# Optimization experiments

Hardware: AMD Instinct MI355X
Metric: run time of the kernel (lower is better)

The kernel has to match this reference:

```python
import jax, jax.numpy as jnp
import numpy as np
import math

B, S, E, H = 2, 2048, 1024, 16
D = E // H  # d_attn = 64
SCALE = 1.0 / math.sqrt(D)


def setup_inputs() -> dict:
    key = jax.random.key(0)
    ks = jax.random.split(key, 5)
    std = 0.02
    return {
        "q": jax.random.normal(ks[0], (B, S, E), dtype=jnp.float32),
        "Wq": jax.random.normal(ks[1], (E, H * D), dtype=jnp.float32) * std,
        "Wk": jax.random.normal(ks[2], (E, H * D), dtype=jnp.float32) * std,
        "Wv": jax.random.normal(ks[3], (E, H * D), dtype=jnp.float32) * std,
        "Wo": jax.random.normal(ks[4], (H * D, E), dtype=jnp.float32) * std,
        "gamma": jnp.ones((H,), dtype=jnp.float32),
    }


def reference(q, Wq, Wk, Wv, Wo, gamma):
    Bq, Sq, _ = q.shape
    # projections -> [B, H, S, D]
    qh = (q @ Wq).reshape(Bq, Sq, H, D).transpose(0, 2, 1, 3)
    kh = (q @ Wk).reshape(Bq, Sq, H, D).transpose(0, 2, 1, 3)
    vh = (q @ Wv).reshape(Bq, Sq, H, D).transpose(0, 2, 1, 3)
    # RBF distance scores: ||q||^2 - 2 q.k + ||k||^2, clamped at 0
    q_norm = jnp.sum(qh * qh, axis=-1, keepdims=True)          # [B,H,S,1]
    k_norm = jnp.sum(kh * kh, axis=-1, keepdims=True)          # [B,H,S,1]
    qk = jnp.einsum("bhsd,bhtd->bhst", qh, kh)                # [B,H,S,S]
    dist = jnp.maximum(q_norm - 2.0 * qk + jnp.swapaxes(k_norm, -2, -1), 0.0)
    scores = jnp.exp(-gamma[None, :, None, None] * SCALE * dist)
    # source: masked_fill(causal_mask == 0, 0) with mask = triu(ones, 1)
    # -> scores kept only on the STRICT upper triangle (faithful to source)
    mask = jnp.triu(jnp.ones((Sq, Sq), dtype=bool), k=1)
    scores = jnp.where(mask, scores, 0.0)
    out = jnp.einsum("bhst,bhtd->bhsd", scores, vh)            # [B,H,S,D]
    out = out.transpose(0, 2, 1, 3).reshape(Bq, Sq, H * D)
    return out @ Wo
```

## Files before the change

### kernel.cpp

```cpp
#include <hip/hip_runtime.h>
#include <stdint.h>

#define SCALE 0.125f
#define GSL_C 0.180336880111f

typedef short s16x8 __attribute__((ext_vector_type(8)));
typedef float f32x4 __attribute__((ext_vector_type(4)));
typedef float f32x16 __attribute__((ext_vector_type(16)));

__device__ __forceinline__ unsigned short f2bf(float x){
  union { float f; unsigned int u; } v; v.f = x;
  unsigned int r = v.u + 0x7fffu + ((v.u >> 16) & 1u);
  return (unsigned short)(r >> 16);
}
__device__ __forceinline__ float bf2f(unsigned short u){
  union { unsigned int u; float f; } v; v.u = ((unsigned int)u) << 16;
  return v.f;
}
__device__ __forceinline__ f32x4 mfma16(s16x8 a, s16x8 b, f32x4 c){
  return __builtin_amdgcn_mfma_f32_16x16x32_bf16(a, b, c, 0, 0, 0);
}
__device__ __forceinline__ f32x16 mfma32(s16x8 a, s16x8 b, f32x16 c){
  return __builtin_amdgcn_mfma_f32_32x32x16_bf16(a, b, c, 0, 0, 0);
}
__device__ __forceinline__ void gld_lds16(const void* g, void* l){
  __builtin_amdgcn_global_load_lds(
      (const __attribute__((address_space(1))) unsigned int*)g,
      (__attribute__((address_space(3))) unsigned int*)l, 16, 0, 0);
}
__device__ __forceinline__ unsigned int cvtpk(float lo, float hi){
  unsigned int r;
  asm("v_cvt_pk_bf16_f32 %0, %1, %2" : "=v"(r) : "v"(lo), "v"(hi));
  return r;
}
__device__ __forceinline__ void plswap(unsigned int &a, unsigned int &b){
  asm("v_permlane32_swap_b32 %0, %1" : "+v"(a), "+v"(b));
}

__global__ __launch_bounds__(256) void prep_kernel(const float* __restrict__ in,
    unsigned short* __restrict__ out,
    const float* __restrict__ W0, const float* __restrict__ W1,
    const float* __restrict__ W2, const float* __restrict__ W3,
    unsigned short* __restrict__ Wt){
  int bid = blockIdx.x;
  int tid = threadIdx.x;
  if (bid < 2048){
    int i = bid*256 + tid;
    const float4* p = (const float4*)in + (size_t)i*2;
    float4 a = p[0], b = p[1];
    unsigned short t[8] = {f2bf(a.x),f2bf(a.y),f2bf(a.z),f2bf(a.w),
                           f2bf(b.x),f2bf(b.y),f2bf(b.z),f2bf(b.w)};
    *(s16x8*)(out + (size_t)i*8) = *(const s16x8*)t;
  } else {
    int idx = bid - 2048;
    int z = idx >> 8, rem = idx & 255;
    int k0 = (rem & 15)*64, n0 = (rem >> 4)*64;
    const float* src = (z==0)?W0:(z==1)?W1:(z==2)?W2:W3;
    unsigned short* dst = Wt + (size_t)z*1048576;
    __shared__ unsigned short tile[64*72];
    int r = tid>>2, c = (tid&3)*16;
    const float* p = src + (size_t)(k0+r)*1024 + n0 + c;
    #pragma unroll
    for (int j=0;j<16;j++) tile[r*72 + c + j] = f2bf(p[j]);
    __syncthreads();
    int n = tid>>2, kc = (tid&3)*16;
    unsigned short o[16];
    #pragma unroll
    for (int j=0;j<16;j++) o[j] = tile[(kc+j)*72 + n];
    *(s16x8*)&dst[(size_t)(n0+n)*1024 + k0 + kc]     = *(const s16x8*)o;
    *(s16x8*)&dst[(size_t)(n0+n)*1024 + k0 + kc + 8] = *(const s16x8*)(o+8);
  }
}

__global__ __launch_bounds__(256) void vtrans_kernel(const unsigned short* __restrict__ Vh,
    unsigned short* __restrict__ VtG){
  int bh = blockIdx.y, t0 = blockIdx.x*64;
  __shared__ unsigned short tile[64*72];
  int tid = threadIdx.x;
  #pragma unroll
  for (int p=0;p<2;p++){
    int idx = p*2048 + tid*8;
    int r = idx>>6, c = idx&63;
    *(s16x8*)&tile[r*72 + c] = *(const s16x8*)&Vh[((size_t)bh*2048 + t0 + r)*64 + c];
  }
  __syncthreads();
  #pragma unroll
  for (int p=0;p<2;p++){
    int idx = p*2048 + tid*8;
    int d = idx>>6, c = idx&63;
    unsigned short o[8];
    #pragma unroll
    for (int j=0;j<8;j++) o[j] = tile[(c+j)*72 + d];
    *(s16x8*)&VtG[((size_t)bh*64 + d)*2048 + t0 + c] = *(const s16x8*)o;
  }
}

template<int MODE>
__global__ __launch_bounds__(512) void gemm_db(const unsigned short* __restrict__ A,
    const unsigned short* __restrict__ Bt, unsigned short* __restrict__ outH,
    float* __restrict__ outF, float* __restrict__ qn, float* __restrict__ kn,
    const float* __restrict__ gamma){
  __shared__ short As[16384];
  __shared__ short Bs[16384];
  int tid = threadIdx.x;
  int w = tid>>6, l = tid&63;
  int lm = l & 15, hi = l >> 4;
  int wr = w>>1, wc = w&1;
  int m0 = blockIdx.x*128, n0 = blockIdx.y*128;

  const unsigned short* Bz;
  int bn0;
  if constexpr (MODE==1){ Bz = Bt + (size_t)(n0>>10)*1048576; bn0 = n0 & 1023; }
  else                  { Bz = Bt; bn0 = n0; }

  f32x4 acc[2][4];
  #pragma unroll
  for (int r=0;r<2;r++)
    #pragma unroll
    for (int c=0;c<4;c++){ f32x4 z = {0.f,0.f,0.f,0.f}; acc[r][c] = z; }

  int rsub = l>>3, csw = ((l&7) ^ (l>>3))*8;
  const unsigned short* gA = A  + (size_t)(m0  + w*16 + rsub)*1024 + csw;
  const unsigned short* gB = Bz + (size_t)(bn0 + w*16 + rsub)*1024 + csw;
  short* lA = As + w*1024;
  short* lB = Bs + w*1024;

  int ch0 = ((hi)     ^ (lm&7))*8;
  int ch1 = ((4 + hi) ^ (lm&7))*8;

  gld_lds16(gA,        lA);
  gld_lds16(gA + 8192, lA + 512);
  gld_lds16(gB,        lB);
  gld_lds16(gB + 8192, lB + 512);
  __syncthreads();

  const int NKT = 16;
  int buf = 0;
  for (int kt=0; kt<NKT; ++kt){
    if (kt+1 < NKT){
      const unsigned short* a = gA + (size_t)(kt+1)*64;
      const unsigned short* b = gB + (size_t)(kt+1)*64;
      short* dA = As + (buf^1)*8192 + w*1024;
      short* dB = Bs + (buf^1)*8192 + w*1024;
      gld_lds16(a,        dA);
      gld_lds16(a + 8192, dA + 512);
      gld_lds16(b,        dB);
      gld_lds16(b + 8192, dB + 512);
    }
    const short* curA = As + buf*8192;
    const short* curB = Bs + buf*8192;
    s16x8 af[2][2], bfv[4][2];
    #pragma unroll
    for (int r=0;r<2;r++){
      int ro = (wr*32 + r*16 + lm)*64;
      af[r][0] = *(const s16x8*)(curA + ro + ch0);
      af[r][1] = *(const s16x8*)(curA + ro + ch1);
    }
    #pragma unroll
    for (int c=0;c<4;c++){
      int ro = (wc*64 + c*16 + lm)*64;
      bfv[c][0] = *(const s16x8*)(curB + ro + ch0);
      bfv[c][1] = *(const s16x8*)(curB + ro + ch1);
    }
    __builtin_amdgcn_s_setprio(1);
    #pragma unroll
    for (int s=0;s<2;s++)
      #pragma unroll
      for (int r=0;r<2;r++)
        #pragma unroll
        for (int c=0;c<4;c++)
          acc[r][c] = mfma16(af[r][s], bfv[c][s], acc[r][c]);
    __builtin_amdgcn_s_setprio(0);
    __syncthreads();
    buf ^= 1;
  }

  if constexpr (MODE==0){
    #pragma unroll
    for (int r=0;r<2;r++)
      #pragma unroll
      for (int c=0;c<4;c++)
        #pragma unroll
        for (int i=0;i<4;i++){
          int m = m0 + wr*32 + r*16 + hi*4 + i;
          int n = n0 + wc*64 + c*16 + lm;
          outF[(size_t)m*1024 + n] = acc[r][c][i];
        }
  } else {
    int z = n0 >> 10;
    unsigned short* oz = outH + (size_t)z*4194304;
    #pragma unroll
    for (int r=0;r<2;r++){
      #pragma unroll
      for (int i=0;i<4;i++){
        int m = m0 + wr*32 + r*16 + hi*4 + i;
        int bq = m >> 11, sq = m & 2047;
        float nrm = 0.f;
        #pragma unroll
        for (int c=0;c<4;c++){
          int nn = (n0 & 1023) + wc*64 + c*16 + lm;
          int hq = nn >> 6, dq = nn & 63;
          int bh = bq*16 + hq;
          unsigned short bv = f2bf(acc[r][c][i]);
          oz[((size_t)bh*2048 + sq)*64 + dq] = bv;
          float vf = bf2f(bv);
          nrm = fmaf(vf, vf, nrm);
        }
        if (z < 2){
          nrm += __shfl_xor(nrm, 1);
          nrm += __shfl_xor(nrm, 2);
          nrm += __shfl_xor(nrm, 4);
          nrm += __shfl_xor(nrm, 8);
          if (lm == 0){
            int hq = ((n0 & 1023) + wc*64) >> 6;
            float gsl_h = gamma[hq] * GSL_C;
            float* dst = z ? kn : qn;
            dst[(size_t)(bq*16 + hq)*2048 + sq] = nrm * gsl_h;
          }
        }
      }
    }
  }
}

__global__ __launch_bounds__(512) void gemm_out(const unsigned short* __restrict__ A,
    const unsigned short* __restrict__ Bt, float* __restrict__ outF){
  __shared__ short As[16384];
  __shared__ short Bs[8192];
  int tid = threadIdx.x;
  int w = tid>>6, l = tid&63;
  int lm = l & 15, hi = l >> 4;
  int wr = w>>1, wc = w&1;
  int m0 = blockIdx.x*128, n0 = blockIdx.y*64;

  f32x4 acc[2][2];
  #pragma unroll
  for (int r=0;r<2;r++)
    #pragma unroll
    for (int c=0;c<2;c++){ f32x4 z = {0.f,0.f,0.f,0.f}; acc[r][c] = z; }

  int rsub = l>>3, csw = ((l&7) ^ (l>>3))*8;
  const unsigned short* gA = A  + (size_t)(m0 + w*16 + rsub)*1024 + csw;
  const unsigned short* gB = Bt + (size_t)(n0 + w*8  + rsub)*1024 + csw;

  int ch0 = ((hi)     ^ (lm&7))*8;
  int ch1 = ((4 + hi) ^ (lm&7))*8;

  gld_lds16(gA,        As + w*1024);
  gld_lds16(gA + 8192, As + w*1024 + 512);
  gld_lds16(gB,        Bs + w*512);
  __syncthreads();

  const int NKT = 16;
  int buf = 0;
  for (int kt=0; kt<NKT; ++kt){
    if (kt+1 < NKT){
      const unsigned short* a = gA + (size_t)(kt+1)*64;
      const unsigned short* b = gB + (size_t)(kt+1)*64;
      gld_lds16(a,        As + (buf^1)*8192 + w*1024);
      gld_lds16(a + 8192, As + (buf^1)*8192 + w*1024 + 512);
      gld_lds16(b,        Bs + (buf^1)*4096 + w*512);
    }
    const short* curA = As + buf*8192;
    const short* curB = Bs + buf*4096;
    s16x8 af[2][2], bfv[2][2];
    #pragma unroll
    for (int r=0;r<2;r++){
      int ro = (wr*32 + r*16 + lm)*64;
      af[r][0] = *(const s16x8*)(curA + ro + ch0);
      af[r][1] = *(const s16x8*)(curA + ro + ch1);
    }
    #pragma unroll
    for (int c=0;c<2;c++){
      int ro = (wc*32 + c*16 + lm)*64;
      bfv[c][0] = *(const s16x8*)(curB + ro + ch0);
      bfv[c][1] = *(const s16x8*)(curB + ro + ch1);
    }
    __builtin_amdgcn_s_setprio(1);
    #pragma unroll
    for (int s=0;s<2;s++)
      #pragma unroll
      for (int r=0;r<2;r++)
        #pragma unroll
        for (int c=0;c<2;c++)
          acc[r][c] = mfma16(af[r][s], bfv[c][s], acc[r][c]);
    __builtin_amdgcn_s_setprio(0);
    __syncthreads();
    buf ^= 1;
  }

  #pragma unroll
  for (int r=0;r<2;r++)
    #pragma unroll
    for (int c=0;c<2;c++)
      #pragma unroll
      for (int i=0;i<4;i++){
        int m = m0 + wr*32 + r*16 + hi*4 + i;
        int n = n0 + wc*32 + c*16 + lm;
        outF[(size_t)m*1024 + n] = acc[r][c][i];
      }
}

#define JOB(si,ts,te,buf,zm) ((unsigned int)((si)|((ts)<<4)|((te)<<10)|((buf)<<16)|((zm)<<18)))
__device__ const unsigned int JOBS[32] = {
  JOB(0,0,11,0,0),   JOB(5,10,21,0,0),  JOB(0,22,32,2,0),  JOB(1,12,22,1,0),
  JOB(2,4,14,0,0),   JOB(6,22,32,1,2),  JOB(2,23,32,2,0),  JOB(7,14,23,0,0),
  JOB(0,11,22,1,0),  JOB(5,21,32,1,2),  JOB(1,2,12,0,0),   JOB(1,22,32,2,0),
  JOB(6,12,22,0,0),  JOB(2,14,23,1,0),  JOB(3,6,15,0,0),   JOB(7,23,32,1,2),
  JOB(11,22,32,0,3), JOB(3,24,32,2,0),  JOB(4,8,16,0,0),   JOB(4,16,24,1,0),
  JOB(4,24,32,2,0),  JOB(8,16,24,0,0),  JOB(3,15,24,1,0),  JOB(8,24,32,1,2),
  JOB(15,30,32,0,3), JOB(14,28,32,0,3), JOB(10,20,26,0,0), JOB(10,26,32,1,2),
  JOB(13,26,32,0,3), JOB(9,18,25,0,0),  JOB(9,25,32,1,2),  JOB(12,24,32,0,3)
};

__global__ __launch_bounds__(256, 4) void attn_kernel(const unsigned short* __restrict__ Qh,
    const unsigned short* __restrict__ Kh, const unsigned short* __restrict__ VtG,
    const float* __restrict__ qn, const float* __restrict__ kn,
    const float* __restrict__ gamma, unsigned short* __restrict__ aO0,
    unsigned short* __restrict__ aO1, unsigned short* __restrict__ aO2){
  __shared__ short Ks[2][4096];
  __shared__ short Vs[2][4096];

  int bid = blockIdx.x;
  int bh = bid & 31; int b = bh>>4, h = bh&15;
  unsigned int e = JOBS[bid >> 5];
  int si2 = e & 15, ts = (e>>4)&63, te = (e>>10)&63, bsel = (e>>16)&3, zm = (e>>18)&3;
  int s0 = si2*128;

  int tid = threadIdx.x, w = tid>>6, l = tid&63;
  int l31 = l & 31, hi5 = l >> 5, l7 = l & 7;
  float gs2l = 2.f * gamma[h] * GSL_C;

  int q0 = s0 + w*32;
  int qrow = q0 + l31;
  const unsigned short* qb = Qh + ((size_t)bh*2048 + qrow)*64;
  s16x8 qf[4];
  #pragma unroll
  for (int c=0;c<4;c++) qf[c] = *(const s16x8*)(qb + c*16 + hi5*8);
  float gq = -qn[(size_t)bh*2048 + qrow];
  const float* knp = kn + (size_t)bh*2048;

  int chs = (l7 ^ (l>>3))*8;
  const unsigned short* kp0 = Kh  + ((size_t)bh*2048 + w*8 + (l>>3))*64 + chs;
  const unsigned short* vp0 = VtG + ((size_t)bh*64 + w*8 + (l>>3))*2048 + chs;

  f32x16 accO0, accO1;
  #pragma unroll
  for (int r=0;r<16;r++){ accO0[r] = 0.f; accO1[r] = 0.f; }

#define STAGE(bufi, tabs) { \
    const unsigned short* kp = kp0 + (size_t)(tabs)*64; \
    const unsigned short* vp = vp0 + (tabs); \
    short* dK = &Ks[bufi][w*512]; \
    short* dV = &Vs[bufi][w*512]; \
    gld_lds16(kp,           dK); \
    gld_lds16(kp + 32*64,   dK + 2048); \
    gld_lds16(vp,           dV); \
    gld_lds16(vp + 32*2048, dV + 2048); \
  }

  STAGE(0, ts*64);
  __syncthreads();

  int cur = 0;
  for (int tt = ts; tt < te; ++tt, cur ^= 1){
    int t0 = tt*64;
    float4 kv[8];
    #pragma unroll
    for (int j=0;j<8;j++) kv[j] = *(const float4*)(knp + t0 + j*8 + hi5*4);
    if (tt + 1 < te) STAGE(cur^1, (tt+1)*64);
    const short* kb = &Ks[cur][0];
    const short* vb = &Vs[cur][0];

    #pragma unroll
    for (int tb=0; tb<2; tb++){
      int tbase = t0 + tb*32 - s0;
      if (tbase + 31 <= w*32) continue;
      f32x16 sc;
      #pragma unroll
      for (int r=0;r<16;r++) sc[r] = 0.f;
      __builtin_amdgcn_s_setprio(1);
      #pragma unroll
      for (int c=0;c<4;c++){
        s16x8 kf = *(const s16x8*)(kb + (tb*32 + l31)*64 + (((2*c + hi5) ^ l7)*8));
        sc = mfma32(kf, qf[c], sc);
      }
      __builtin_amdgcn_s_setprio(0);
      float ev[16];
      #pragma unroll
      for (int gg=0; gg<4; gg++){
        float4 knv = kv[tb*4 + gg];
        float ks4[4] = {knv.x, knv.y, knv.z, knv.w};
        #pragma unroll
        for (int i=0;i<4;i++){
          int r = gg*4 + i;
          ev[r] = __builtin_amdgcn_exp2f(fminf(fmaf(gs2l, sc[r], gq - ks4[i]), 0.f));
        }
      }
      if (tbase < w*32 + 32){
        #pragma unroll
        for (int r=0;r<16;r++){
          int t = t0 + tb*32 + (r&3) + 8*(r>>2) + 4*hi5;
          ev[r] = (t > qrow) ? ev[r] : 0.f;
        }
      }
      unsigned int u0 = cvtpk(ev[0],  ev[1]),  u1 = cvtpk(ev[2],  ev[3]);
      unsigned int u2 = cvtpk(ev[4],  ev[5]),  u3 = cvtpk(ev[6],  ev[7]);
      unsigned int u4 = cvtpk(ev[8],  ev[9]),  u5 = cvtpk(ev[10], ev[11]);
      unsigned int u6 = cvtpk(ev[12], ev[13]), u7 = cvtpk(ev[14], ev[15]);
      plswap(u0, u2);
      plswap(u1, u3);
      plswap(u4, u6);
      plswap(u5, u7);
      unsigned int f0[4] = {u0, u1, u2, u3};
      unsigned int f1[4] = {u4, u5, u6, u7};
      s16x8 pa0 = *(const s16x8*)f0;
      s16x8 pa1 = *(const s16x8*)f1;
      __builtin_amdgcn_s_setprio(1);
      {
        int cg0 = 2*tb, cg1 = 2*tb + 1;
        s16x8 v00 = *(const s16x8*)(vb + (l31)*64      + (((2*cg0 + hi5) ^ l7)*8));
        s16x8 v01 = *(const s16x8*)(vb + (l31)*64      + (((2*cg1 + hi5) ^ l7)*8));
        s16x8 v10 = *(const s16x8*)(vb + (32 + l31)*64 + (((2*cg0 + hi5) ^ l7)*8));
        s16x8 v11 = *(const s16x8*)(vb + (32 + l31)*64 + (((2*cg1 + hi5) ^ l7)*8));
        accO0 = mfma32(pa0, v00, accO0);
        accO0 = mfma32(pa1, v01, accO0);
        accO1 = mfma32(pa0, v10, accO1);
        accO1 = mfma32(pa1, v11, accO1);
      }
      __builtin_amdgcn_s_setprio(0);
    }
    __syncthreads();
  }
#undef STAGE

  unsigned short* aoP = (bsel==0) ? aO0 : (bsel==1) ? aO1 : aO2;
  #pragma unroll
  for (int r=0;r<16;r++){
    int s = q0 + (r&3) + 8*(r>>2) + 4*hi5;
    size_t base = ((size_t)b*2048 + s)*1024 + h*64;
    aoP[base + l31]      = f2bf(accO0[r]);
    aoP[base + 32 + l31] = f2bf(accO1[r]);
  }
  if (zm){
    s16x8 zz8 = {0,0,0,0,0,0,0,0};
    int zr = tid >> 1, zc = (tid & 1)*32;
    size_t zbase = ((size_t)b*2048 + s0 + zr)*1024 + h*64 + zc;
    if (zm & 1){
      #pragma unroll
      for (int j=0;j<4;j++) *(s16x8*)&aO1[zbase + j*8] = zz8;
    }
    if (zm & 2){
      #pragma unroll
      for (int j=0;j<4;j++) *(s16x8*)&aO2[zbase + j*8] = zz8;
    }
  }
}

__global__ __launch_bounds__(256) void sum3_kernel(unsigned short* __restrict__ a,
    const unsigned short* __restrict__ bsrc, const unsigned short* __restrict__ csrc){
  size_t i = ((size_t)blockIdx.x*256 + threadIdx.x)*8;
  s16x8 va = *(const s16x8*)(a + i);
  s16x8 vb = *(const s16x8*)(bsrc + i);
  s16x8 vc = *(const s16x8*)(csrc + i);
  unsigned short o[8];
  #pragma unroll
  for (int j=0;j<8;j++)
    o[j] = f2bf(bf2f((unsigned short)va[j]) + bf2f((unsigned short)vb[j])
                + bf2f((unsigned short)vc[j]));
  *(s16x8*)(a + i) = *(const s16x8*)o;
}

extern "C" void kernel_launch(void* const* d_in, const int* in_sizes, int n_in,
                              void* d_out, int out_size, void* d_ws, size_t ws_size,
                              hipStream_t stream){
  const float* q  = (const float*)d_in[0];
  const float* Wq = (const float*)d_in[1];
  const float* Wk = (const float*)d_in[2];
  const float* Wv = (const float*)d_in[3];
  const float* Wo = (const float*)d_in[4];
  const float* gm = (const float*)d_in[5];
  float* out = (float*)d_out;

  unsigned short* qbf = (unsigned short*)d_ws;
  unsigned short* Wt  = qbf + 4194304;
  unsigned short* Qh  = Wt  + 4194304;
  unsigned short* Kh  = Qh  + 4194304;
  unsigned short* Vh  = Kh  + 4194304;
  unsigned short* Vt  = Vh  + 4194304;
  unsigned short* aO  = Vt  + 4194304;
  float* qn = (float*)(aO + 4194304);
  float* kn = qn + 65536;

  unsigned short* aO1 = qbf;
  unsigned short* aO2 = Vh;

  prep_kernel  <<<dim3(3072), 256, 0, stream>>>(q, qbf, Wq, Wk, Wv, Wo, Wt);
  gemm_db<1>   <<<dim3(32,24), 512, 0, stream>>>(qbf, Wt, Qh, nullptr, qn, kn, gm);
  vtrans_kernel<<<dim3(32,32), 256, 0, stream>>>(Vh, Vt);
  attn_kernel  <<<dim3(1024), 256, 0, stream>>>(Qh, Kh, Vt, qn, kn, gm, aO, aO1, aO2);
  sum3_kernel  <<<dim3(2048), 256, 0, stream>>>(aO, aO1, aO2);
  gemm_out     <<<dim3(32,16), 512, 0, stream>>>(aO, Wt + 3*1048576, out);
}
```

Measured before the change: 106.1 us.

## Fuse partial-sum reduction into output GEMM and rework projection GEMM with 32x32 MFMA split-K

Removes the separate sum3 kernel by having gemm_out load the three bf16 partial attention outputs, sum them in registers, and write the result into LDS while the MFMAs for the current tile run. The projection GEMM is rewritten to use 32x32x16 MFMAs with a two-way intra-block split-K across warp groups, reduced through LDS before the bf16 store and norm computation. This saves a kernel launch and one full read/write pass over the attention output, and should improve MFMA efficiency in the projection GEMM. In exchange it adds register pressure, an extra LDS exchange and sync, and non-async global loads in the output GEMM's A path.

```diff
diff --git a/kernel.cpp b/kernel.cpp
--- a/kernel.cpp
+++ b/kernel.cpp
@@ -95,135 +95,131 @@
   }
 }
 
-template<int MODE>
-__global__ __launch_bounds__(512) void gemm_db(const unsigned short* __restrict__ A,
+__global__ __launch_bounds__(512, 4) void gemm_proj(const unsigned short* __restrict__ A,
     const unsigned short* __restrict__ Bt, unsigned short* __restrict__ outH,
-    float* __restrict__ outF, float* __restrict__ qn, float* __restrict__ kn,
-    const float* __restrict__ gamma){
-  __shared__ short As[16384];
-  __shared__ short Bs[16384];
+    float* __restrict__ qn, float* __restrict__ kn, const float* __restrict__ gamma){
+  __shared__ short As[2][8192];
+  __shared__ short Bs[2][8192];
   int tid = threadIdx.x;
   int w = tid>>6, l = tid&63;
-  int lm = l & 15, hi = l >> 4;
-  int wr = w>>1, wc = w&1;
+  int l31 = l & 31, hi5 = l >> 5;
+  int wm = (w>>1)&1, wn = w&1, ks = w>>2, pid = w&3;
   int m0 = blockIdx.x*128, n0 = blockIdx.y*128;
-
-  const unsigned short* Bz;
-  int bn0;
-  if constexpr (MODE==1){ Bz = Bt + (size_t)(n0>>10)*1048576; bn0 = n0 & 1023; }
-  else                  { Bz = Bt; bn0 = n0; }
-
-  f32x4 acc[2][4];
-  #pragma unroll
-  for (int r=0;r<2;r++)
-    #pragma unroll
-    for (int c=0;c<4;c++){ f32x4 z = {0.f,0.f,0.f,0.f}; acc[r][c] = z; }
-
-  int rsub = l>>3, csw = ((l&7) ^ (l>>3))*8;
+  int z = n0 >> 10, bn0 = n0 & 1023;
+  const unsigned short* Bz = Bt + (size_t)z*1048576;
+
+  f32x16 acc[2][2];
+  #pragma unroll
+  for (int mh=0;mh<2;mh++)
+    #pragma unroll
+    for (int nh=0;nh<2;nh++)
+      #pragma unroll
+      for (int r=0;r<16;r++) acc[mh][nh][r] = 0.f;
+
+  int rsub = l>>3, csw = ((l&7) ^ rsub)*8;
   const unsigned short* gA = A  + (size_t)(m0  + w*16 + rsub)*1024 + csw;
   const unsigned short* gB = Bz + (size_t)(bn0 + w*16 + rsub)*1024 + csw;
-  short* lA = As + w*1024;
-  short* lB = Bs + w*1024;
-
-  int ch0 = ((hi)     ^ (lm&7))*8;
-  int ch1 = ((4 + hi) ^ (lm&7))*8;
-
-  gld_lds16(gA,        lA);
-  gld_lds16(gA + 8192, lA + 512);
-  gld_lds16(gB,        lB);
-  gld_lds16(gB + 8192, lB + 512);
+
+  int ch0 = ((4*ks + hi5)     ^ (l31&7))*8;
+  int ch1 = ((4*ks + 2 + hi5) ^ (l31&7))*8;
+
+  gld_lds16(gA,        &As[0][w*1024]);
+  gld_lds16(gA + 8192, &As[0][w*1024 + 512]);
+  gld_lds16(gB,        &Bs[0][w*1024]);
+  gld_lds16(gB + 8192, &Bs[0][w*1024 + 512]);
   __syncthreads();
 
-  const int NKT = 16;
   int buf = 0;
-  for (int kt=0; kt<NKT; ++kt){
-    if (kt+1 < NKT){
+  #pragma unroll 1
+  for (int kt=0; kt<16; ++kt){
+    if (kt+1 < 16){
       const unsigned short* a = gA + (size_t)(kt+1)*64;
       const unsigned short* b = gB + (size_t)(kt+1)*64;
-      short* dA = As + (buf^1)*8192 + w*1024;
-      short* dB = Bs + (buf^1)*8192 + w*1024;
-      gld_lds16(a,        dA);
-      gld_lds16(a + 8192, dA + 512);
-      gld_lds16(b,        dB);
-      gld_lds16(b + 8192, dB + 512);
-    }
-    const short* curA = As + buf*8192;
-    const short* curB = Bs + buf*8192;
-    s16x8 af[2][2], bfv[4][2];
-    #pragma unroll
-    for (int r=0;r<2;r++){
-      int ro = (wr*32 + r*16 + lm)*64;
-      af[r][0] = *(const s16x8*)(curA + ro + ch0);
-      af[r][1] = *(const s16x8*)(curA + ro + ch1);
-    }
-    #pragma unroll
-    for (int c=0;c<4;c++){
-      int ro = (wc*64 + c*16 + lm)*64;
-      bfv[c][0] = *(const s16x8*)(curB + ro + ch0);
-      bfv[c][1] = *(const s16x8*)(curB + ro + ch1);
+      gld_lds16(a,        &As[buf^1][w*1024]);
+      gld_lds16(a + 8192, &As[buf^1][w*1024 + 512]);
+      gld_lds16(b,        &Bs[buf^1][w*1024]);
+      gld_lds16(b + 8192, &Bs[buf^1][w*1024 + 512]);
+    }
+    const short* cA = &As[buf][0];
+    const short* cB = &Bs[buf][0];
+    s16x8 af[2][2], bfv[2][2];
+    #pragma unroll
+    for (int mh=0;mh<2;mh++){
+      int ro = (wm*64 + mh*32 + l31)*64;
+      af[mh][0] = *(const s16x8*)(cA + ro + ch0);
+      af[mh][1] = *(const s16x8*)(cA + ro + ch1);
+    }
+    #pragma unroll
+    for (int nh=0;nh<2;nh++){
+      int ro = (wn*64 + nh*32 + l31)*64;
+      bfv[nh][0] = *(const s16x8*)(cB + ro + ch0);
+      bfv[nh][1] = *(const s16x8*)(cB + ro + ch1);
     }
     __builtin_amdgcn_s_setprio(1);
     #pragma unroll
-    for (int s=0;s<2;s++)
-      #pragma unroll
-      for (int r=0;r<2;r++)
+    for (int ci=0;ci<2;ci++)
+      #pragma unroll
+      for (int mh=0;mh<2;mh++)
         #pragma unroll
-        for (int c=0;c<4;c++)
-          acc[r][c] = mfma16(af[r][s], bfv[c][s], acc[r][c]);
+        for (int nh=0;nh<2;nh++)
+          acc[mh][nh] = mfma32(af[mh][ci], bfv[nh][ci], acc[mh][nh]);
     __builtin_amdgcn_s_setprio(0);
     __syncthreads();
     buf ^= 1;
   }
 
-  if constexpr (MODE==0){
-    #pragma unroll
-    for (int r=0;r<2;r++)
-      #pragma unroll
-      for (int c=0;c<4;c++)
+  float* xch = (pid < 2) ? ((float*)&As[0][0] + (size_t)pid*4096)
+                         : ((float*)&Bs[0][0] + (size_t)(pid-2)*4096);
+  if (ks == 1){
+    #pragma unroll
+    for (int mh=0;mh<2;mh++)
+      #pragma unroll
+      for (int nh=0;nh<2;nh++)
+        *(f32x16*)(xch + (mh*2+nh)*1024 + l*16) = acc[mh][nh];
+  }
+  __syncthreads();
+  if (ks == 0){
+    #pragma unroll
+    for (int mh=0;mh<2;mh++)
+      #pragma unroll
+      for (int nh=0;nh<2;nh++){
+        f32x16 o = *(const f32x16*)(xch + (mh*2+nh)*1024 + l*16);
         #pragma unroll
-        for (int i=0;i<4;i++){
-          int m = m0 + wr*32 + r*16 + hi*4 + i;
-          int n = n0 + wc*64 + c*16 + lm;
-          outF[(size_t)m*1024 + n] = acc[r][c][i];
-        }
-  } else {
-    int z = n0 >> 10;
+        for (int r=0;r<16;r++) acc[mh][nh][r] += o[r];
+      }
     unsigned short* oz = outH + (size_t)z*4194304;
-    #pragma unroll
-    for (int r=0;r<2;r++){
-      #pragma unroll
-      for (int i=0;i<4;i++){
-        int m = m0 + wr*32 + r*16 + hi*4 + i;
+    int hq = (bn0 + wn*64) >> 6;
+    float gsl_h = (z < 2) ? gamma[hq]*GSL_C : 0.f;
+    float* dst = z ? kn : qn;
+    #pragma unroll
+    for (int mh=0;mh<2;mh++){
+      #pragma unroll
+      for (int r=0;r<16;r++){
+        int m = m0 + wm*64 + mh*32 + (r&3) + 8*(r>>2) + 4*hi5;
         int bq = m >> 11, sq = m & 2047;
-        float nrm = 0.f;
-        #pragma unroll
-        for (int c=0;c<4;c++){
-          int nn = (n0 & 1023) + wc*64 + c*16 + lm;
-          int hq = nn >> 6, dq = nn & 63;
-          int bh = bq*16 + hq;
-          unsigned short bv = f2bf(acc[r][c][i]);
-          oz[((size_t)bh*2048 + sq)*64 + dq] = bv;
-          float vf = bf2f(bv);
-          nrm = fmaf(vf, vf, nrm);
-        }
+        int bh = bq*16 + hq;
+        unsigned short b0 = f2bf(acc[mh][0][r]);
+        unsigned short b1 = f2bf(acc[mh][1][r]);
+        size_t rowb = ((size_t)bh*2048 + sq)*64;
+        oz[rowb + l31]      = b0;
+        oz[rowb + 32 + l31] = b1;
         if (z < 2){
+          float v0 = bf2f(b0), v1 = bf2f(b1);
+          float nrm = v0*v0 + v1*v1;
           nrm += __shfl_xor(nrm, 1);
           nrm += __shfl_xor(nrm, 2);
           nrm += __shfl_xor(nrm, 4);
           nrm += __shfl_xor(nrm, 8);
-          if (lm == 0){
-            int hq = ((n0 & 1023) + wc*64) >> 6;
-            float gsl_h = gamma[hq] * GSL_C;
-            float* dst = z ? kn : qn;
-            dst[(size_t)(bq*16 + hq)*2048 + sq] = nrm * gsl_h;
-          }
+          nrm += __shfl_xor(nrm, 16);
+          if (l31 == 0) dst[(size_t)bh*2048 + sq] = nrm * gsl_h;
         }
       }
     }
   }
 }
 
-__global__ __launch_bounds__(512) void gemm_out(const unsigned short* __restrict__ A,
+__global__ __launch_bounds__(512) void gemm_out(const unsigned short* __restrict__ A0,
+    const unsigned short* __restrict__ A1, const unsigned short* __restrict__ A2,
     const unsigned short* __restrict__ Bt, float* __restrict__ outF){
   __shared__ short As[16384];
   __shared__ short Bs[8192];
@@ -237,29 +233,41 @@
   #pragma unroll
   for (int r=0;r<2;r++)
     #pragma unroll
-    for (int c=0;c<2;c++){ f32x4 z = {0.f,0.f,0.f,0.f}; acc[r][c] = z; }
-
-  int rsub = l>>3, csw = ((l&7) ^ (l>>3))*8;
-  const unsigned short* gA = A  + (size_t)(m0 + w*16 + rsub)*1024 + csw;
-  const unsigned short* gB = Bt + (size_t)(n0 + w*8  + rsub)*1024 + csw;
+    for (int c=0;c<2;c++){ f32x4 zz = {0.f,0.f,0.f,0.f}; acc[r][c] = zz; }
+
+  int rsub = l>>3, csw = ((l&7) ^ rsub)*8;
+  size_t aoff0 = (size_t)(m0 + w*16 + rsub)*1024 + csw;
+  const unsigned short* gB = Bt + (size_t)(n0 + w*8 + rsub)*1024 + csw;
 
   int ch0 = ((hi)     ^ (lm&7))*8;
   int ch1 = ((4 + hi) ^ (lm&7))*8;
 
-  gld_lds16(gA,        As + w*1024);
-  gld_lds16(gA + 8192, As + w*1024 + 512);
-  gld_lds16(gB,        Bs + w*512);
+  gld_lds16(gB, Bs + w*512);
+  {
+    size_t o0 = aoff0, o1 = aoff0 + 8192;
+    s16x8 va0 = *(const s16x8*)(A0+o0), vb0 = *(const s16x8*)(A1+o0), vc0 = *(const s16x8*)(A2+o0);
+    s16x8 va1 = *(const s16x8*)(A0+o1), vb1 = *(const s16x8*)(A1+o1), vc1 = *(const s16x8*)(A2+o1);
+    unsigned short t0[8], t1[8];
+    #pragma unroll
+    for (int e=0;e<8;e++){
+      t0[e] = f2bf(bf2f((unsigned short)va0[e]) + bf2f((unsigned short)vb0[e]) + bf2f((unsigned short)vc0[e]));
+      t1[e] = f2bf(bf2f((unsigned short)va1[e]) + bf2f((unsigned short)vb1[e]) + bf2f((unsigned short)vc1[e]));
+    }
+    *(s16x8*)(As + w*1024 + l*8)       = *(const s16x8*)t0;
+    *(s16x8*)(As + w*1024 + 512 + l*8) = *(const s16x8*)t1;
+  }
   __syncthreads();
 
-  const int NKT = 16;
   int buf = 0;
-  for (int kt=0; kt<NKT; ++kt){
-    if (kt+1 < NKT){
-      const unsigned short* a = gA + (size_t)(kt+1)*64;
-      const unsigned short* b = gB + (size_t)(kt+1)*64;
-      gld_lds16(a,        As + (buf^1)*8192 + w*1024);
-      gld_lds16(a + 8192, As + (buf^1)*8192 + w*1024 + 512);
-      gld_lds16(b,        Bs + (buf^1)*4096 + w*512);
+  #pragma unroll 1
+  for (int kt=0; kt<16; ++kt){
+    s16x8 va0, vb0, vc0, va1, vb1, vc1;
+    bool pre = (kt+1 < 16);
+    if (pre){
+      gld_lds16(gB + (size_t)(kt+1)*64, Bs + (buf^1)*4096 + w*512);
+      size_t o0 = aoff0 + (size_t)(kt+1)*64, o1 = o0 + 8192;
+      va0 = *(const s16x8*)(A0+o0); vb0 = *(const s16x8*)(A1+o0); vc0 = *(const s16x8*)(A2+o0);
+      va1 = *(const s16x8*)(A0+o1); vb1 = *(const s16x8*)(A1+o1); vc1 = *(const s16x8*)(A2+o1);
     }
     const short* curA = As + buf*8192;
     const short* curB = Bs + buf*4096;
@@ -285,6 +293,16 @@
         for (int c=0;c<2;c++)
           acc[r][c] = mfma16(af[r][s], bfv[c][s], acc[r][c]);
     __builtin_amdgcn_s_setprio(0);
+    if (pre){
+      unsigned short t0[8], t1[8];
+      #pragma unroll
+      for (int e=0;e<8;e++){
+        t0[e] = f2bf(bf2f((unsigned short)va0[e]) + bf2f((unsigned short)vb0[e]) + bf2f((unsigned short)vc0[e]));
+        t1[e] = f2bf(bf2f((unsigned short)va1[e]) + bf2f((unsigned short)vb1[e]) + bf2f((unsigned short)vc1[e]));
+      }
+      *(s16x8*)(As + (buf^1)*8192 + w*1024 + l*8)       = *(const s16x8*)t0;
+      *(s16x8*)(As + (buf^1)*8192 + w*1024 + 512 + l*8) = *(const s16x8*)t1;
+    }
     __syncthreads();
     buf ^= 1;
   }
@@ -457,20 +475,6 @@
   }
 }
 
-__global__ __launch_bounds__(256) void sum3_kernel(unsigned short* __restrict__ a,
-    const unsigned short* __restrict__ bsrc, const unsigned short* __restrict__ csrc){
-  size_t i = ((size_t)blockIdx.x*256 + threadIdx.x)*8;
-  s16x8 va = *(const s16x8*)(a + i);
-  s16x8 vb = *(const s16x8*)(bsrc + i);
-  s16x8 vc = *(const s16x8*)(csrc + i);
-  unsigned short o[8];
-  #pragma unroll
-  for (int j=0;j<8;j++)
-    o[j] = f2bf(bf2f((unsigned short)va[j]) + bf2f((unsigned short)vb[j])
-                + bf2f((unsigned short)vc[j]));
-  *(s16x8*)(a + i) = *(const s16x8*)o;
-}
-
 extern "C" void kernel_launch(void* const* d_in, const int* in_sizes, int n_in,
                               void* d_out, int out_size, void* d_ws, size_t ws_size,
                               hipStream_t stream){
@@ -496,9 +500,8 @@
   unsigned short* aO2 = Vh;
 
   prep_kernel  <<<dim3(3072), 256, 0, stream>>>(q, qbf, Wq, Wk, Wv, Wo, Wt);
-  gemm_db<1>   <<<dim3(32,24), 512, 0, stream>>>(qbf, Wt, Qh, nullptr, qn, kn, gm);
+  gemm_proj    <<<dim3(32,24), 512, 0, stream>>>(qbf, Wt, Qh, qn, kn, gm);
   vtrans_kernel<<<dim3(32,32), 256, 0, stream>>>(Vh, Vt);
   attn_kernel  <<<dim3(1024), 256, 0, stream>>>(Qh, Kh, Vt, qn, kn, gm, aO, aO1, aO2);
-  sum3_kernel  <<<dim3(2048), 256, 0, stream>>>(aO, aO1, aO2);
-  gemm_out     <<<dim3(32,16), 512, 0, stream>>>(aO, Wt + 3*1048576, out);
-}
+  gemm_out     <<<dim3(32,16), 512, 0, stream>>>(aO, aO1, aO2, Wt + 3*1048576, out);
+}
```

Result: slower. 126.7 us (+19.4%).

## Drop LDS staging in attention; read K and V straight from global

Applied to the files above, without the earlier changes.

The attention kernel no longer double-buffers K and V tiles through shared memory with async global-to-LDS loads and per-tile barriers. Each wave now loads its K rows and transposed-V fragments directly from global memory, relying on L1/L2 cache for reuse across the four waves. This removes LDS traffic and __syncthreads, but it loses the explicit prefetch overlap and multiplies global/cache load traffic, since all waves fetch the same K/V data. The projection GEMM is also de-templated into a single-mode function, which is cleanup only.

```diff
diff --git a/kernel.cpp b/kernel.cpp
--- a/kernel.cpp
+++ b/kernel.cpp
@@ -95,11 +95,9 @@
   }
 }
 
-template<int MODE>
-__global__ __launch_bounds__(512) void gemm_db(const unsigned short* __restrict__ A,
+__global__ __launch_bounds__(512) void gemm_proj(const unsigned short* __restrict__ A,
     const unsigned short* __restrict__ Bt, unsigned short* __restrict__ outH,
-    float* __restrict__ outF, float* __restrict__ qn, float* __restrict__ kn,
-    const float* __restrict__ gamma){
+    float* __restrict__ qn, float* __restrict__ kn, const float* __restrict__ gamma){
   __shared__ short As[16384];
   __shared__ short Bs[16384];
   int tid = threadIdx.x;
@@ -108,10 +106,8 @@
   int wr = w>>1, wc = w&1;
   int m0 = blockIdx.x*128, n0 = blockIdx.y*128;
 
-  const unsigned short* Bz;
-  int bn0;
-  if constexpr (MODE==1){ Bz = Bt + (size_t)(n0>>10)*1048576; bn0 = n0 & 1023; }
-  else                  { Bz = Bt; bn0 = n0; }
+  const unsigned short* Bz = Bt + (size_t)(n0>>10)*1048576;
+  int bn0 = n0 & 1023;
 
   f32x4 acc[2][4];
   #pragma unroll
@@ -175,48 +171,35 @@
     buf ^= 1;
   }
 
-  if constexpr (MODE==0){
-    #pragma unroll
-    for (int r=0;r<2;r++)
-      #pragma unroll
-      for (int c=0;c<4;c++)
-        #pragma unroll
-        for (int i=0;i<4;i++){
-          int m = m0 + wr*32 + r*16 + hi*4 + i;
-          int n = n0 + wc*64 + c*16 + lm;
-          outF[(size_t)m*1024 + n] = acc[r][c][i];
-        }
-  } else {
-    int z = n0 >> 10;
-    unsigned short* oz = outH + (size_t)z*4194304;
-    #pragma unroll
-    for (int r=0;r<2;r++){
-      #pragma unroll
-      for (int i=0;i<4;i++){
-        int m = m0 + wr*32 + r*16 + hi*4 + i;
-        int bq = m >> 11, sq = m & 2047;
-        float nrm = 0.f;
-        #pragma unroll
-        for (int c=0;c<4;c++){
-          int nn = (n0 & 1023) + wc*64 + c*16 + lm;
-          int hq = nn >> 6, dq = nn & 63;
-          int bh = bq*16 + hq;
-          unsigned short bv = f2bf(acc[r][c][i]);
-          oz[((size_t)bh*2048 + sq)*64 + dq] = bv;
-          float vf = bf2f(bv);
-          nrm = fmaf(vf, vf, nrm);
-        }
-        if (z < 2){
-          nrm += __shfl_xor(nrm, 1);
-          nrm += __shfl_xor(nrm, 2);
-          nrm += __shfl_xor(nrm, 4);
-          nrm += __shfl_xor(nrm, 8);
-          if (lm == 0){
-            int hq = ((n0 & 1023) + wc*64) >> 6;
-            float gsl_h = gamma[hq] * GSL_C;
-            float* dst = z ? kn : qn;
-            dst[(size_t)(bq*16 + hq)*2048 + sq] = nrm * gsl_h;
-          }
+  int z = n0 >> 10;
+  unsigned short* oz = outH + (size_t)z*4194304;
+  #pragma unroll
+  for (int r=0;r<2;r++){
+    #pragma unroll
+    for (int i=0;i<4;i++){
+      int m = m0 + wr*32 + r*16 + hi*4 + i;
+      int bq = m >> 11, sq = m & 2047;
+      float nrm = 0.f;
+      #pragma unroll
+      for (int c=0;c<4;c++){
+        int nn = bn0 + wc*64 + c*16 + lm;
+        int hq = nn >> 6, dq = nn & 63;
+        int bh = bq*16 + hq;
+        unsigned short bv = f2bf(acc[r][c][i]);
+        oz[((size_t)bh*2048 + sq)*64 + dq] = bv;
+        float vf = bf2f(bv);
+        nrm = fmaf(vf, vf, nrm);
+      }
+      if (z < 2){
+        nrm += __shfl_xor(nrm, 1);
+        nrm += __shfl_xor(nrm, 2);
+        nrm += __shfl_xor(nrm, 4);
+        nrm += __shfl_xor(nrm, 8);
+        if (lm == 0){
+          int hq = (bn0 + wc*64) >> 6;
+          float gsl_h = gamma[hq] * GSL_C;
+          float* dst = z ? kn : qn;
+          dst[(size_t)(bq*16 + hq)*2048 + sq] = nrm * gsl_h;
         }
       }
     }
@@ -318,9 +301,6 @@
     const float* __restrict__ qn, const float* __restrict__ kn,
     const float* __restrict__ gamma, unsigned short* __restrict__ aO0,
     unsigned short* __restrict__ aO1, unsigned short* __restrict__ aO2){
-  __shared__ short Ks[2][4096];
-  __shared__ short Vs[2][4096];
-
   int bid = blockIdx.x;
   int bh = bid & 31; int b = bh>>4, h = bh&15;
   unsigned int e = JOBS[bid >> 5];
@@ -328,7 +308,7 @@
   int s0 = si2*128;
 
   int tid = threadIdx.x, w = tid>>6, l = tid&63;
-  int l31 = l & 31, hi5 = l >> 5, l7 = l & 7;
+  int l31 = l & 31, hi5 = l >> 5;
   float gs2l = 2.f * gamma[h] * GSL_C;
 
   int q0 = s0 + w*32;
@@ -340,56 +320,34 @@
   float gq = -qn[(size_t)bh*2048 + qrow];
   const float* knp = kn + (size_t)bh*2048;
 
-  int chs = (l7 ^ (l>>3))*8;
-  const unsigned short* kp0 = Kh  + ((size_t)bh*2048 + w*8 + (l>>3))*64 + chs;
-  const unsigned short* vp0 = VtG + ((size_t)bh*64 + w*8 + (l>>3))*2048 + chs;
+  const unsigned short* kbase = Kh  + (size_t)bh*131072;
+  const unsigned short* vbase = VtG + (size_t)bh*131072;
 
   f32x16 accO0, accO1;
   #pragma unroll
   for (int r=0;r<16;r++){ accO0[r] = 0.f; accO1[r] = 0.f; }
 
-#define STAGE(bufi, tabs) { \
-    const unsigned short* kp = kp0 + (size_t)(tabs)*64; \
-    const unsigned short* vp = vp0 + (tabs); \
-    short* dK = &Ks[bufi][w*512]; \
-    short* dV = &Vs[bufi][w*512]; \
-    gld_lds16(kp,           dK); \
-    gld_lds16(kp + 32*64,   dK + 2048); \
-    gld_lds16(vp,           dV); \
-    gld_lds16(vp + 32*2048, dV + 2048); \
-  }
-
-  STAGE(0, ts*64);
-  __syncthreads();
-
-  int cur = 0;
-  for (int tt = ts; tt < te; ++tt, cur ^= 1){
+  for (int tt = ts; tt < te; ++tt){
     int t0 = tt*64;
-    float4 kv[8];
-    #pragma unroll
-    for (int j=0;j<8;j++) kv[j] = *(const float4*)(knp + t0 + j*8 + hi5*4);
-    if (tt + 1 < te) STAGE(cur^1, (tt+1)*64);
-    const short* kb = &Ks[cur][0];
-    const short* vb = &Vs[cur][0];
-
     #pragma unroll
     for (int tb=0; tb<2; tb++){
       int tbase = t0 + tb*32 - s0;
       if (tbase + 31 <= w*32) continue;
+      const unsigned short* kr = kbase + (size_t)(t0 + tb*32 + l31)*64 + hi5*8;
       f32x16 sc;
       #pragma unroll
       for (int r=0;r<16;r++) sc[r] = 0.f;
       __builtin_amdgcn_s_setprio(1);
       #pragma unroll
       for (int c=0;c<4;c++){
-        s16x8 kf = *(const s16x8*)(kb + (tb*32 + l31)*64 + (((2*c + hi5) ^ l7)*8));
+        s16x8 kf = *(const s16x8*)(kr + c*16);
         sc = mfma32(kf, qf[c], sc);
       }
       __builtin_amdgcn_s_setprio(0);
       float ev[16];
       #pragma unroll
       for (int gg=0; gg<4; gg++){
-        float4 knv = kv[tb*4 + gg];
+        float4 knv = *(const float4*)(knp + t0 + tb*32 + gg*8 + hi5*4);
         float ks4[4] = {knv.x, knv.y, knv.z, knv.w};
         #pragma unroll
         for (int i=0;i<4;i++){
@@ -416,23 +374,20 @@
       unsigned int f1[4] = {u4, u5, u6, u7};
       s16x8 pa0 = *(const s16x8*)f0;
       s16x8 pa1 = *(const s16x8*)f1;
+      const unsigned short* vr0 = vbase + (size_t)l31*2048 + t0 + tb*32 + hi5*8;
+      const unsigned short* vr1 = vr0 + 32*2048;
+      s16x8 v00 = *(const s16x8*)(vr0);
+      s16x8 v01 = *(const s16x8*)(vr0 + 16);
+      s16x8 v10 = *(const s16x8*)(vr1);
+      s16x8 v11 = *(const s16x8*)(vr1 + 16);
       __builtin_amdgcn_s_setprio(1);
-      {
-        int cg0 = 2*tb, cg1 = 2*tb + 1;
-        s16x8 v00 = *(const s16x8*)(vb + (l31)*64      + (((2*cg0 + hi5) ^ l7)*8));
-        s16x8 v01 = *(const s16x8*)(vb + (l31)*64      + (((2*cg1 + hi5) ^ l7)*8));
-        s16x8 v10 = *(const s16x8*)(vb + (32 + l31)*64 + (((2*cg0 + hi5) ^ l7)*8));
-        s16x8 v11 = *(const s16x8*)(vb + (32 + l31)*64 + (((2*cg1 + hi5) ^ l7)*8));
-        accO0 = mfma32(pa0, v00, accO0);
-        accO0 = mfma32(pa1, v01, accO0);
-        accO1 = mfma32(pa0, v10, accO1);
-        accO1 = mfma32(pa1, v11, accO1);
-      }
+      accO0 = mfma32(pa0, v00, accO0);
+      accO0 = mfma32(pa1, v01, accO0);
+      accO1 = mfma32(pa0, v10, accO1);
+      accO1 = mfma32(pa1, v11, accO1);
       __builtin_amdgcn_s_setprio(0);
     }
-    __syncthreads();
-  }
-#undef STAGE
+  }
 
   unsigned short* aoP = (bsel==0) ? aO0 : (bsel==1) ? aO1 : aO2;
   #pragma unroll
@@ -496,7 +451,7 @@
   unsigned short* aO2 = Vh;
 
   prep_kernel  <<<dim3(3072), 256, 0, stream>>>(q, qbf, Wq, Wk, Wv, Wo, Wt);
-  gemm_db<1>   <<<dim3(32,24), 512, 0, stream>>>(qbf, Wt, Qh, nullptr, qn, kn, gm);
+  gemm_proj    <<<dim3(32,24), 512, 0, stream>>>(qbf, Wt, Qh, qn, kn, gm);
   vtrans_kernel<<<dim3(32,32), 256, 0, stream>>>(Vh, Vt);
   attn_kernel  <<<dim3(1024), 256, 0, stream>>>(Qh, Kh, Vt, qn, kn, gm, aO, aO1, aO2);
   sum3_kernel  <<<dim3(2048), 256, 0, stream>>>(aO, aO1, aO2);
```

Measured after the change: 146.4 us. 37.9% more time.
